# Performance work log

Measured on AMD Instinct MI355X. Metric: run time of the kernel, lower is better.

## Reference

```python
import jax, jax.numpy as jnp
import numpy as np
from jax import lax

SDIM = 30
DIM = SDIM * SDIM          # 900
SPECTRAL_RADIUS = 0.9
LEAKY = 0.7
TRAIN_LEN = 30000
DISCARD = 1000
T = TRAIN_LEN + DISCARD    # 31000 sequential steps


def setup_inputs() -> dict:
    key = jax.random.key(0)
    kW, kWin, ku = jax.random.split(key, 3)
    # W: random symmetric matrix normalized by max |eigenvalue| (as in __init__ via eigvalsh)
    A = np.asarray(jax.random.normal(kW, (DIM, DIM), dtype=jnp.float32))
    A = (A + A.T) * 0.5
    A = A / np.max(np.abs(np.linalg.eigvalsh(A)))
    W = jnp.asarray(A, dtype=jnp.float32)
    # W_in: uniform in (-1, 1)
    W_in = jax.random.uniform(kWin, (DIM, DIM), dtype=jnp.float32, minval=-1.0, maxval=1.0)
    # scalar input series, scaled to (-0.2, 0.2) like MinMaxScaler in the driver
    u = jax.random.uniform(ku, (T,), dtype=jnp.float32, minval=-0.2, maxval=0.2)
    return {"W": W, "W_in": W_in, "u": u}


def reference(W, W_in, u):
    # forward(): u (scalar) is zero-padded to length DIM with u at index 0,
    # so W_in @ u_pad == W_in[:, 0] * u.
    w_eff = SPECTRAL_RADIUS * W        # [DIM, DIM]
    win0 = W_in[:, 0]                  # [DIM]
    leaky = jnp.float32(LEAKY)

    def step(x, ut):
        x_new = (1.0 - leaky) * x + leaky * jnp.tanh(w_eff @ x + win0 * ut)
        return x_new, x_new

    x0 = jnp.zeros((DIM,), dtype=W.dtype)
    _, xs = lax.scan(step, x0, u)      # xs: [T, DIM], xs[i] = state after step i
    # collect_states appends for i > DISCARD, then stacks and transposes
    states = xs[DISCARD + 1:].T        # [DIM, TRAIN_LEN - 1] = [900, 29999]
    return states
```

## Files before the change

kernel.cpp:

```cpp
#include <hip/hip_runtime.h>
#include <math.h>


#define DIM        900
#define T_TOTAL    31000
#define DISCARD_P1 1001
#define OUT_T      29999
#define NBLK       60
#define ROWS_PB    15
#define NTHREADS   256
#define SR         0.9f
#define LEAKY      0.7f
#define RING_W     64

#define XBUF_F    1024
#define WS_INIT_N 2048

typedef float vfloat4 __attribute__((ext_vector_type(4)));

__global__ void esn_init_ws(float* ws) {
    int i = threadIdx.x + blockIdx.x * blockDim.x;
    if (i < WS_INIT_N) ws[i] = 0.0f;
}

__device__ __forceinline__ void store_line16(float* p, vfloat4 v) {
    asm volatile("global_store_dwordx4 %0, %1, off sc0 sc1"
                 :: "v"(p), "v"(v) : "memory");
}

#define POLL_ISSUE(reg, srcp)                                        \
    asm volatile("global_load_dwordx4 %0, %1, off sc0 sc1"           \
                 : "=v"(reg) : "v"(srcp) : "memory")

__launch_bounds__(NTHREADS, 1)
__global__ void esn_persistent(const float* __restrict__ W,
                               const float* __restrict__ W_in,
                               const float* __restrict__ u,
                               float* __restrict__ out,
                               float* xbuf)
{
    __shared__ float x_lds[1024];
    __shared__ float ring[ROWS_PB][RING_W + 1];
    __shared__ float res[16];

    const int tid   = threadIdx.x;
    const int blk   = blockIdx.x;
    const int row0  = blk * ROWS_PB;
    const int wave  = tid >> 6;
    const int lane  = tid & 63;
    const int rbase = wave * 4;

    for (int i = tid; i < 1024; i += NTHREADS) x_lds[i] = 0.0f;

    vfloat4 wreg[4][4];
    #pragma unroll
    for (int r = 0; r < 4; ++r) {
        const int row = rbase + r;
        #pragma unroll
        for (int k = 0; k < 4; ++k) {
            const int p = 4 * lane + 256 * k;
            vfloat4 v = (vfloat4)0.0f;
            if (row < ROWS_PB) {
                #pragma unroll
                for (int j = 0; j < 4; ++j) {
                    const int pp  = p + j;
                    const int off = pp & 15;
                    if (pp < 960 && off < 15) {
                        const int col = (pp >> 4) * 15 + off;
                        v[j] = SR * W[(size_t)(row0 + row) * DIM + col];
                    }
                }
            }
            wreg[r][k] = v;
        }
    }
    float win0r = 0.0f;
    if (lane < 4 && rbase + lane < ROWS_PB)
        win0r = W_in[(size_t)(row0 + rbase + lane) * DIM];

    const int  sidx    = wave * 15 + (lane >> 2);
    const int  chunk   = lane & 3;
    const bool taglane = (lane < 60) && (chunk == 3);

    vfloat4 v0, v1;

    __syncthreads();

    for (int s = 0; s < T_TOTAL; ++s) {
        const float ut  = u[s];
        const float tag = (float)s;
        const float* xin = xbuf + (size_t)(s & 1) * XBUF_F;

        if (lane < 60) {
            const float* src = xin + sidx * 16 + chunk * 4;
            float* dst = &x_lds[sidx * 16 + chunk * 4];
            POLL_ISSUE(v0, src);
            for (;;) {
                POLL_ISSUE(v1, src);
                asm volatile("s_waitcnt vmcnt(1)"
                             : "+v"(v0) :: "memory");
                if (__all(!taglane || (v0.w == tag))) {
                    *reinterpret_cast<vfloat4*>(dst) = v0;
                    break;
                }
                POLL_ISSUE(v0, src);
                asm volatile("s_waitcnt vmcnt(1)"
                             : "+v"(v1) :: "memory");
                if (__all(!taglane || (v1.w == tag))) {
                    *reinterpret_cast<vfloat4*>(dst) = v1;
                    break;
                }
            }
        }
        __syncthreads();

        float a0 = 0.f, a1 = 0.f, a2 = 0.f, a3 = 0.f;
        #pragma unroll
        for (int k = 0; k < 4; ++k) {
            const vfloat4 xv =
                *reinterpret_cast<const vfloat4*>(&x_lds[4 * lane + 256 * k]);
            a0 += wreg[0][k].x * xv.x + wreg[0][k].y * xv.y
                + wreg[0][k].z * xv.z + wreg[0][k].w * xv.w;
            a1 += wreg[1][k].x * xv.x + wreg[1][k].y * xv.y
                + wreg[1][k].z * xv.z + wreg[1][k].w * xv.w;
            a2 += wreg[2][k].x * xv.x + wreg[2][k].y * xv.y
                + wreg[2][k].z * xv.z + wreg[2][k].w * xv.w;
            a3 += wreg[3][k].x * xv.x + wreg[3][k].y * xv.y
                + wreg[3][k].z * xv.z + wreg[3][k].w * xv.w;
        }

        a0 += __shfl_xor(a0, 1, 64);
        a1 += __shfl_xor(a1, 1, 64);
        a2 += __shfl_xor(a2, 1, 64);
        a3 += __shfl_xor(a3, 1, 64);
        float m01 = (lane & 1) ? a1 : a0;
        float m23 = (lane & 1) ? a3 : a2;
        m01 += __shfl_xor(m01, 2, 64);
        m23 += __shfl_xor(m23, 2, 64);
        float m = (lane & 2) ? m23 : m01;
        #pragma unroll
        for (int off = 4; off < 64; off <<= 1)
            m += __shfl_xor(m, off, 64);

        if (lane < 4) {
            const int r = rbase + lane;
            if (r < ROWS_PB) {
                float z = m + win0r * ut;
                z = fminf(fmaxf(z, -9.0f), 9.0f);
                const float e  = __expf(2.0f * z);
                const float th = (e - 1.0f) / (e + 1.0f);
                const float xn = (1.0f - LEAKY) * x_lds[blk * 16 + r]
                               + LEAKY * th;
                res[r] = xn;
                if (s >= DISCARD_P1)
                    ring[r][(s - DISCARD_P1) & (RING_W - 1)] = xn;
            } else {
                res[15] = (float)(s + 1);
            }
        }
        __syncthreads();

        if (tid < 4) {
            const vfloat4 rv =
                *reinterpret_cast<const vfloat4*>(&res[4 * tid]);
            store_line16(xbuf + (size_t)((s + 1) & 1) * XBUF_F
                              + (size_t)blk * 16 + 4 * tid, rv);
        }

        if (s >= DISCARD_P1) {
            const int  c    = s - DISCARD_P1;
            const bool last = (s == T_TOTAL - 1);
            if ((c & (RING_W - 1)) == (RING_W - 1) || last) {
                const int len = (c & (RING_W - 1)) + 1;
                const int c0  = c - len + 1;
                if (len == RING_W) {
                    for (int i = tid; i < ROWS_PB * RING_W; i += NTHREADS) {
                        const int row = i >> 6, col = i & (RING_W - 1);
                        out[(size_t)(row0 + row) * OUT_T + c0 + col] =
                            ring[row][col];
                    }
                } else {
                    for (int i = tid; i < ROWS_PB * len; i += NTHREADS) {
                        const int row = i / len, col = i % len;
                        out[(size_t)(row0 + row) * OUT_T + c0 + col] =
                            ring[row][col];
                    }
                }
            }
        }

        if (wave == 0)
            asm volatile("s_waitcnt vmcnt(1)"
                         : "+v"(v0), "+v"(v1) :: "memory");
        else
            asm volatile("s_waitcnt vmcnt(0)"
                         : "+v"(v0), "+v"(v1) :: "memory");
    }
}

extern "C" void kernel_launch(void* const* d_in, const int* in_sizes, int n_in,
                              void* d_out, int out_size, void* d_ws, size_t ws_size,
                              hipStream_t stream) {
    const float* W    = (const float*)d_in[0];
    const float* W_in = (const float*)d_in[1];
    const float* u    = (const float*)d_in[2];
    float* out = (float*)d_out;
    float* ws  = (float*)d_ws;

    esn_init_ws<<<WS_INIT_N / 256, 256, 0, stream>>>(ws);
    esn_persistent<<<NBLK, NTHREADS, 0, stream>>>(W, W_in, u, out, ws);
}
```

Before: 49.97 ms.

## Poll full state vector directly into registers per wave, drop LDS staging barrier

Each wave now polls the entire 960-float state buffer from global memory into registers with four vector loads per lane, instead of 60 lanes cooperatively loading it into LDS followed by a block barrier. This removes one __syncthreads and the LDS round trip per time step from the critical serial path. The own-row previous state is kept in a double-buffered shared res array instead of the LDS copy of x. The cost is four times more polling traffic per block, since every wave reads the whole vector, and more registers per lane.

```diff
diff --git a/kernel.cpp b/kernel.cpp
--- a/kernel.cpp
+++ b/kernel.cpp
@@ -28,9 +28,23 @@
                  :: "v"(p), "v"(v) : "memory");
 }
 
-#define POLL_ISSUE(reg, srcp)                                        \
-    asm volatile("global_load_dwordx4 %0, %1, off sc0 sc1"           \
-                 : "=v"(reg) : "v"(srcp) : "memory")
+#define POLL_SET(c0, c1, c2, c3, srcp)                                  \
+    asm volatile("global_load_dwordx4 %0, %4, off sc0 sc1\n\t"          \
+                 "global_load_dwordx4 %1, %4, off offset:1024 sc0 sc1\n\t" \
+                 "global_load_dwordx4 %2, %4, off offset:2048 sc0 sc1\n\t" \
+                 "global_load_dwordx4 %3, %4, off offset:3072 sc0 sc1"  \
+                 : "=v"(c0), "=v"(c1), "=v"(c2), "=v"(c3)               \
+                 : "v"(srcp) : "memory")
+
+#define WAIT_SET(c0, c1, c2, c3)                                        \
+    asm volatile("s_waitcnt vmcnt(4)"                                   \
+                 : "+v"(c0), "+v"(c1), "+v"(c2), "+v"(c3) :: "memory")
+
+#define TAG_OK(c0, c1, c2, c3, okvar)                                   \
+    { bool ok_ = true;                                                  \
+      if (lt)  ok_ = (c0.w == tag) & (c1.w == tag) & (c2.w == tag);     \
+      if (t3v) ok_ = ok_ & (c3.w == tag);                               \
+      okvar = __all(ok_); }
 
 __launch_bounds__(NTHREADS, 1)
 __global__ void esn_persistent(const float* __restrict__ W,
@@ -39,9 +53,8 @@
                                float* __restrict__ out,
                                float* xbuf)
 {
-    __shared__ float x_lds[1024];
     __shared__ float ring[ROWS_PB][RING_W + 1];
-    __shared__ float res[16];
+    __shared__ __align__(16) float res[2][16];
 
     const int tid   = threadIdx.x;
     const int blk   = blockIdx.x;
@@ -49,8 +62,6 @@
     const int wave  = tid >> 6;
     const int lane  = tid & 63;
     const int rbase = wave * 4;
-
-    for (int i = tid; i < 1024; i += NTHREADS) x_lds[i] = 0.0f;
 
     vfloat4 wreg[4][4];
     #pragma unroll
@@ -78,56 +89,66 @@
     if (lane < 4 && rbase + lane < ROWS_PB)
         win0r = W_in[(size_t)(row0 + rbase + lane) * DIM];
 
-    const int  sidx    = wave * 15 + (lane >> 2);
-    const int  chunk   = lane & 3;
-    const bool taglane = (lane < 60) && (chunk == 3);
-
-    vfloat4 v0, v1;
-
+    const bool lt  = (lane & 3) == 3;
+    const bool t3v = lt && ((lane >> 2) < 12);
+
+    if (lane < 4) { res[0][rbase + lane] = 0.0f; res[1][rbase + lane] = 0.0f; }
     __syncthreads();
+
+    vfloat4 A0, A1, A2, A3, B0, B1, B2, B3;
 
     for (int s = 0; s < T_TOTAL; ++s) {
         const float ut  = u[s];
         const float tag = (float)s;
-        const float* xin = xbuf + (size_t)(s & 1) * XBUF_F;
-
-        if (lane < 60) {
-            const float* src = xin + sidx * 16 + chunk * 4;
-            float* dst = &x_lds[sidx * 16 + chunk * 4];
-            POLL_ISSUE(v0, src);
-            for (;;) {
-                POLL_ISSUE(v1, src);
-                asm volatile("s_waitcnt vmcnt(1)"
-                             : "+v"(v0) :: "memory");
-                if (__all(!taglane || (v0.w == tag))) {
-                    *reinterpret_cast<vfloat4*>(dst) = v0;
-                    break;
-                }
-                POLL_ISSUE(v0, src);
-                asm volatile("s_waitcnt vmcnt(1)"
-                             : "+v"(v1) :: "memory");
-                if (__all(!taglane || (v1.w == tag))) {
-                    *reinterpret_cast<vfloat4*>(dst) = v1;
-                    break;
-                }
-            }
-        }
-        __syncthreads();
-
-        float a0 = 0.f, a1 = 0.f, a2 = 0.f, a3 = 0.f;
-        #pragma unroll
-        for (int k = 0; k < 4; ++k) {
-            const vfloat4 xv =
-                *reinterpret_cast<const vfloat4*>(&x_lds[4 * lane + 256 * k]);
-            a0 += wreg[0][k].x * xv.x + wreg[0][k].y * xv.y
-                + wreg[0][k].z * xv.z + wreg[0][k].w * xv.w;
-            a1 += wreg[1][k].x * xv.x + wreg[1][k].y * xv.y
-                + wreg[1][k].z * xv.z + wreg[1][k].w * xv.w;
-            a2 += wreg[2][k].x * xv.x + wreg[2][k].y * xv.y
-                + wreg[2][k].z * xv.z + wreg[2][k].w * xv.w;
-            a3 += wreg[3][k].x * xv.x + wreg[3][k].y * xv.y
-                + wreg[3][k].z * xv.z + wreg[3][k].w * xv.w;
-        }
+        const float* src = xbuf + (size_t)(s & 1) * XBUF_F + 4 * lane;
+
+        vfloat4 xv0, xv1, xv2, xv3;
+        POLL_SET(A0, A1, A2, A3, src);
+        for (;;) {
+            POLL_SET(B0, B1, B2, B3, src);
+            WAIT_SET(A0, A1, A2, A3);
+            bool ok;
+            TAG_OK(A0, A1, A2, A3, ok);
+            if (ok) { xv0 = A0; xv1 = A1; xv2 = A2; xv3 = A3; break; }
+            POLL_SET(A0, A1, A2, A3, src);
+            WAIT_SET(B0, B1, B2, B3);
+            TAG_OK(B0, B1, B2, B3, ok);
+            if (ok) { xv0 = B0; xv1 = B1; xv2 = B2; xv3 = B3; break; }
+        }
+
+        float a0, a1, a2, a3;
+        a0  = wreg[0][0].x * xv0.x + wreg[0][0].y * xv0.y
+            + wreg[0][0].z * xv0.z + wreg[0][0].w * xv0.w;
+        a1  = wreg[1][0].x * xv0.x + wreg[1][0].y * xv0.y
+            + wreg[1][0].z * xv0.z + wreg[1][0].w * xv0.w;
+        a2  = wreg[2][0].x * xv0.x + wreg[2][0].y * xv0.y
+            + wreg[2][0].z * xv0.z + wreg[2][0].w * xv0.w;
+        a3  = wreg[3][0].x * xv0.x + wreg[3][0].y * xv0.y
+            + wreg[3][0].z * xv0.z + wreg[3][0].w * xv0.w;
+        a0 += wreg[0][1].x * xv1.x + wreg[0][1].y * xv1.y
+            + wreg[0][1].z * xv1.z + wreg[0][1].w * xv1.w;
+        a1 += wreg[1][1].x * xv1.x + wreg[1][1].y * xv1.y
+            + wreg[1][1].z * xv1.z + wreg[1][1].w * xv1.w;
+        a2 += wreg[2][1].x * xv1.x + wreg[2][1].y * xv1.y
+            + wreg[2][1].z * xv1.z + wreg[2][1].w * xv1.w;
+        a3 += wreg[3][1].x * xv1.x + wreg[3][1].y * xv1.y
+            + wreg[3][1].z * xv1.z + wreg[3][1].w * xv1.w;
+        a0 += wreg[0][2].x * xv2.x + wreg[0][2].y * xv2.y
+            + wreg[0][2].z * xv2.z + wreg[0][2].w * xv2.w;
+        a1 += wreg[1][2].x * xv2.x + wreg[1][2].y * xv2.y
+            + wreg[1][2].z * xv2.z + wreg[1][2].w * xv2.w;
+        a2 += wreg[2][2].x * xv2.x + wreg[2][2].y * xv2.y
+            + wreg[2][2].z * xv2.z + wreg[2][2].w * xv2.w;
+        a3 += wreg[3][2].x * xv2.x + wreg[3][2].y * xv2.y
+            + wreg[3][2].z * xv2.z + wreg[3][2].w * xv2.w;
+        a0 += wreg[0][3].x * xv3.x + wreg[0][3].y * xv3.y
+            + wreg[0][3].z * xv3.z + wreg[0][3].w * xv3.w;
+        a1 += wreg[1][3].x * xv3.x + wreg[1][3].y * xv3.y
+            + wreg[1][3].z * xv3.z + wreg[1][3].w * xv3.w;
+        a2 += wreg[2][3].x * xv3.x + wreg[2][3].y * xv3.y
+            + wreg[2][3].z * xv3.z + wreg[2][3].w * xv3.w;
+        a3 += wreg[3][3].x * xv3.x + wreg[3][3].y * xv3.y
+            + wreg[3][3].z * xv3.z + wreg[3][3].w * xv3.w;
 
         a0 += __shfl_xor(a0, 1, 64);
         a1 += __shfl_xor(a1, 1, 64);
@@ -144,25 +165,26 @@
 
         if (lane < 4) {
             const int r = rbase + lane;
+            float* resp = res[(s + 1) & 1];
             if (r < ROWS_PB) {
                 float z = m + win0r * ut;
                 z = fminf(fmaxf(z, -9.0f), 9.0f);
                 const float e  = __expf(2.0f * z);
                 const float th = (e - 1.0f) / (e + 1.0f);
-                const float xn = (1.0f - LEAKY) * x_lds[blk * 16 + r]
-                               + LEAKY * th;
-                res[r] = xn;
+                const float xo = res[s & 1][r];
+                const float xn = (1.0f - LEAKY) * xo + LEAKY * th;
+                resp[r] = xn;
                 if (s >= DISCARD_P1)
                     ring[r][(s - DISCARD_P1) & (RING_W - 1)] = xn;
             } else {
-                res[15] = (float)(s + 1);
+                resp[15] = (float)(s + 1);
             }
         }
         __syncthreads();
 
         if (tid < 4) {
             const vfloat4 rv =
-                *reinterpret_cast<const vfloat4*>(&res[4 * tid]);
+                *reinterpret_cast<const vfloat4*>(&res[(s + 1) & 1][4 * tid]);
             store_line16(xbuf + (size_t)((s + 1) & 1) * XBUF_F
                               + (size_t)blk * 16 + 4 * tid, rv);
         }
@@ -191,10 +213,12 @@
 
         if (wave == 0)
             asm volatile("s_waitcnt vmcnt(1)"
-                         : "+v"(v0), "+v"(v1) :: "memory");
+                         : "+v"(A0), "+v"(A1), "+v"(A2), "+v"(A3),
+                           "+v"(B0), "+v"(B1), "+v"(B2), "+v"(B3) :: "memory");
         else
             asm volatile("s_waitcnt vmcnt(0)"
-                         : "+v"(v0), "+v"(v1) :: "memory");
+                         : "+v"(A0), "+v"(A1), "+v"(A2), "+v"(A3),
+                           "+v"(B0), "+v"(B1), "+v"(B2), "+v"(B3) :: "memory");
     }
 }
 
```

Measured after the change: 52.55 ms. 1.05x slower.
